# Optimization experiments

Hardware: AMD Instinct MI355X
Metric: run time of the kernel (lower is better)

Reference implementation:

```python
import jax, jax.numpy as jnp
import numpy as np

T, D_IN, D, H, A = 8192, 2048, 512, 512, 18  # seq_len, obs_dim, dense_size, cell_size, action_size


def setup_inputs() -> dict:
    key = jax.random.key(0)
    ks = jax.random.split(key, 12)
    g = lambda k, sh, s: (jax.random.normal(k, sh, jnp.float32) * s)
    return {
        "x": g(ks[0], (T, D_IN), 1.0),
        "prev_hidden": jnp.zeros((1, H), jnp.float32),
        "W1": g(ks[1], (D_IN, D), 0.02), "b1": jnp.zeros((D,), jnp.float32),
        "W2": g(ks[2], (D, D), 0.04),    "b2": jnp.zeros((D,), jnp.float32),
        "Wg": g(ks[3], (D, 3 * H), 0.04),   # GRU input kernel [D, 3H] (z|r|h)
        "Ug": g(ks[4], (H, 3 * H), 0.04),   # GRU recurrent kernel [H, 3H]
        "bg": jnp.zeros((2, 3 * H), jnp.float32),  # reset_after=True: input + recurrent bias
        "Wp": g(ks[5], (H, A), 0.05), "bp": jnp.zeros((A,), jnp.float32),
        "Wv": g(ks[6], (H, 1), 0.05), "bv": jnp.zeros((1,), jnp.float32),
    }


def reference(x, prev_hidden, W1, b1, W2, b2, Wg, Ug, bg, Wp, bp, Wv, bv):
    # MLP front-end (relu)
    z = jax.nn.relu(x @ W1 + b1)
    z = jax.nn.relu(z @ W2 + b2)
    # Precompute input projections for all timesteps: [T, 3H]
    X = z @ Wg + bg[0]
    b_rec = bg[1]

    def step(h, xt):  # h: [1,H], xt: [3H]
        rec = h @ Ug + b_rec                    # [1, 3H]
        xz, xr, xh = jnp.split(xt, 3)           # each [H]
        rz, rr, rh = jnp.split(rec, 3, axis=1)  # each [1, H]
        zt = jax.nn.sigmoid(xz + rz)
        rt = jax.nn.sigmoid(xr + rr)
        hh = jax.nn.sigmoid(xh + rt * rh)       # activation='sigmoid' (candidate)
        hn = zt * h + (1.0 - zt) * hh
        return hn, hn[0]

    hT, seq = jax.lax.scan(step, prev_hidden, X)  # seq: [T, H]
    policy = jax.nn.softmax(seq @ Wp + bp, axis=-1)
    value = seq @ Wv + bv
    return policy, value, hT
```

## Files before the change

### kernel.cpp

```cpp
#include <hip/hip_runtime.h>
#include <hip/hip_bf16.h>


#define T_STEPS 8192
#define DIN 2048
#define DD 512
#define HHH 512
#define AACT 18
#define H3 1536
#define NWG 32

typedef __attribute__((ext_vector_type(8))) short short8;
typedef __attribute__((ext_vector_type(4))) float f32x4;

__global__ void cast_f32_bf16(const float* __restrict__ in,
                              __hip_bfloat16* __restrict__ out, int n)
{
    int i = blockIdx.x * 256 + threadIdx.x;
    if (i < n) out[i] = __float2bfloat16(in[i]);
}

__global__ void init_ctl(int* ctl) { ctl[0] = 0; ctl[1] = 0; ctl[2] = 0; }

__global__ __launch_bounds__(256) void gemm_bf16(
    const float* __restrict__ A32, const __hip_bfloat16* __restrict__ A16,
    const __hip_bfloat16* __restrict__ B, const float* __restrict__ bias,
    __hip_bfloat16* __restrict__ Cb, float* __restrict__ Cf,
    int M, int N, int K, int relu)
{
    const int m0 = blockIdx.x * 64;
    const int n0 = blockIdx.y * 64;
    const int t  = threadIdx.x;
    const int wave = t >> 6;
    const int lane = t & 63;
    const int quad = lane >> 4;
    const int l16  = lane & 15;

    __shared__ __align__(16) __hip_bfloat16 As[64 * 40];
    __shared__ __align__(16) __hip_bfloat16 Bs[64 * 40];

    f32x4 acc[4];
#pragma unroll
    for (int c = 0; c < 4; ++c) acc[c] = (f32x4){0.f, 0.f, 0.f, 0.f};

    const int ar = t >> 2, akc = (t & 3) * 8;
    const int bk = t >> 3, bn  = (t & 7) * 8;

    for (int kb = 0; kb < K; kb += 32) {
        if (A32) {
            const float* src = A32 + (size_t)(m0 + ar) * K + kb + akc;
            float4 f0 = *(const float4*)(src);
            float4 f1 = *(const float4*)(src + 4);
            union { short8 v; __hip_bfloat16 h[8]; } u;
            u.h[0] = __float2bfloat16(f0.x); u.h[1] = __float2bfloat16(f0.y);
            u.h[2] = __float2bfloat16(f0.z); u.h[3] = __float2bfloat16(f0.w);
            u.h[4] = __float2bfloat16(f1.x); u.h[5] = __float2bfloat16(f1.y);
            u.h[6] = __float2bfloat16(f1.z); u.h[7] = __float2bfloat16(f1.w);
            *(short8*)&As[ar * 40 + akc] = u.v;
        } else {
            const __hip_bfloat16* src = A16 + (size_t)(m0 + ar) * K + kb + akc;
            *(short8*)&As[ar * 40 + akc] = *(const short8*)src;
        }
        {
            const __hip_bfloat16* src = B + (size_t)(kb + bk) * N + n0 + bn;
            short8 v = *(const short8*)src;
            const __hip_bfloat16* vh = (const __hip_bfloat16*)&v;
#pragma unroll
            for (int i = 0; i < 8; ++i) Bs[(bn + i) * 40 + bk] = vh[i];
        }
        __syncthreads();

        short8 a = *(const short8*)&As[(wave * 16 + l16) * 40 + quad * 8];
#pragma unroll
        for (int c = 0; c < 4; ++c) {
            short8 b = *(const short8*)&Bs[(c * 16 + l16) * 40 + quad * 8];
            acc[c] = __builtin_amdgcn_mfma_f32_16x16x32_bf16(a, b, acc[c], 0, 0, 0);
        }
        __syncthreads();
    }

#pragma unroll
    for (int c = 0; c < 4; ++c) {
        const int col = n0 + c * 16 + l16;
        const float bb = bias ? bias[col] : 0.f;
#pragma unroll
        for (int r = 0; r < 4; ++r) {
            const int row = m0 + wave * 16 + quad * 4 + r;
            float v = acc[c][r] + bb;
            if (relu) v = fmaxf(v, 0.f);
            if (Cb) Cb[(size_t)row * N + col] = __float2bfloat16(v);
            if (Cf) Cf[(size_t)row * N + col] = v;
        }
    }
}

template <int CTRL>
__device__ __forceinline__ float dpp_red_add(float x)
{
    int sh = __builtin_amdgcn_update_dpp(0, __float_as_int(x), CTRL, 0xF, 0xF, true);
    return x + __int_as_float(sh);
}

__device__ __forceinline__ void wg_barrier_lds_only()
{
    asm volatile("s_waitcnt lgkmcnt(0)" ::: "memory");
    __builtin_amdgcn_s_barrier();
    asm volatile("" ::: "memory");
}

__global__ __launch_bounds__(256)
__attribute__((amdgpu_waves_per_eu(1, 1)))
void scan_kernel(
    const float* __restrict__ X,
    const float* __restrict__ Ug,
    const float* __restrict__ bg,
    const float* __restrict__ h0,
    float* __restrict__ seq,
    unsigned long long* __restrict__ hbuf,
    float* __restrict__ hT,
    int* __restrict__ ctl)
{
    const int t  = threadIdx.x;
    const int wg = blockIdx.x;
    const int jl = t >> 4;
    const int kp = t & 15;
    const int j  = wg * 16 + jl;
    const int k0 = kp * 32;

    __shared__ __align__(16) float h_lds[2][16 * 36];
    __shared__ int wg_abort;
    if (t == 0) wg_abort = 0;

    float wz[32], wr[32], wh[32];
#pragma unroll
    for (int m = 0; m < 32; ++m) {
        const float* row = Ug + (size_t)(k0 + m) * H3;
        wz[m] = row[j];
        wr[m] = row[512 + j];
        wh[m] = row[1024 + j];
    }
#pragma unroll
    for (int m = 0; m < 32; ++m) {
        asm volatile("" : "+a"(wz[m]), "+a"(wr[m]), "+a"(wh[m]));
    }

    const float* brec = bg + H3;
    const float bz = brec[j], brr = brec[512 + j], bh = brec[1024 + j];
    float hj = h0[j];

    const int k1 = t, k2 = t + 256;
    const int la1 = (k1 >> 5) * 36 + (k1 & 31);
    const int la2 = (k2 >> 5) * 36 + (k2 & 31);

    float xz = 0.f, xr = 0.f, xh = 0.f;
    if (kp == 0) { xz = X[j]; xr = X[512 + j]; xh = X[1024 + j]; }

    for (int s = 0; s < T_STEPS; ++s) {
        float* hl = h_lds[s & 1];

        float nxz = 0.f, nxr = 0.f, nxh = 0.f;
        if (kp == 0 && s + 1 < T_STEPS) {
            const float* Xs = X + (size_t)(s + 1) * H3;
            nxz = Xs[j]; nxr = Xs[512 + j]; nxh = Xs[1024 + j];
        }

        if (s == 0) {
            hl[la1] = h0[k1];
            hl[la2] = h0[k2];
        } else {
            const unsigned long long* src = hbuf + ((size_t)(s & 1) << 9);
            unsigned long long v1 = 0, v2 = 0;
            unsigned long long a1 = __hip_atomic_load(src + k1, __ATOMIC_RELAXED, __HIP_MEMORY_SCOPE_AGENT);
            unsigned long long a2 = __hip_atomic_load(src + k2, __ATOMIC_RELAXED, __HIP_MEMORY_SCOPE_AGENT);
            asm volatile("" ::: "memory");
            __builtin_amdgcn_s_sleep(4);
            asm volatile("" ::: "memory");
            unsigned long long b1 = __hip_atomic_load(src + k1, __ATOMIC_RELAXED, __HIP_MEMORY_SCOPE_AGENT);
            unsigned long long b2 = __hip_atomic_load(src + k2, __ATOMIC_RELAXED, __HIP_MEMORY_SCOPE_AGENT);
            bool ok1 = false, ok2 = false;
            int guard = 0;
            for (;;) {
                if (!ok1 && (unsigned)(a1 >> 32) == (unsigned)s) { v1 = a1; ok1 = true; }
                if (!ok2 && (unsigned)(a2 >> 32) == (unsigned)s) { v2 = a2; ok2 = true; }
                if (ok1 && ok2) break;
                if (!ok1) a1 = __hip_atomic_load(src + k1, __ATOMIC_RELAXED, __HIP_MEMORY_SCOPE_AGENT);
                if (!ok2) a2 = __hip_atomic_load(src + k2, __ATOMIC_RELAXED, __HIP_MEMORY_SCOPE_AGENT);
                if (!ok1 && (unsigned)(b1 >> 32) == (unsigned)s) { v1 = b1; ok1 = true; }
                if (!ok2 && (unsigned)(b2 >> 32) == (unsigned)s) { v2 = b2; ok2 = true; }
                if (ok1 && ok2) break;
                if (!ok1) b1 = __hip_atomic_load(src + k1, __ATOMIC_RELAXED, __HIP_MEMORY_SCOPE_AGENT);
                if (!ok2) b2 = __hip_atomic_load(src + k2, __ATOMIC_RELAXED, __HIP_MEMORY_SCOPE_AGENT);
                if ((++guard & 511) == 0) {
                    int ab = __hip_atomic_load(ctl + 2, __ATOMIC_RELAXED,
                                               __HIP_MEMORY_SCOPE_AGENT);
                    if (ab || guard > (1 << 16)) {
                        wg_abort = 1;
                        __hip_atomic_store(ctl + 2, 1, __ATOMIC_RELAXED,
                                           __HIP_MEMORY_SCOPE_AGENT);
                        break;
                    }
                }
            }
            hl[la1] = __uint_as_float((unsigned)v1);
            hl[la2] = __uint_as_float((unsigned)v2);
        }
        wg_barrier_lds_only();
        if (wg_abort) return;

        float accz = 0.f, accr = 0.f, acch = 0.f;
        const float* hb = &hl[kp * 36];
#pragma unroll
        for (int m = 0; m < 32; m += 4) {
            float4 hv = *(const float4*)(hb + m);
            accz = fmaf(hv.x, wz[m    ], accz);
            accz = fmaf(hv.y, wz[m + 1], accz);
            accz = fmaf(hv.z, wz[m + 2], accz);
            accz = fmaf(hv.w, wz[m + 3], accz);
            accr = fmaf(hv.x, wr[m    ], accr);
            accr = fmaf(hv.y, wr[m + 1], accr);
            accr = fmaf(hv.z, wr[m + 2], accr);
            accr = fmaf(hv.w, wr[m + 3], accr);
            acch = fmaf(hv.x, wh[m    ], acch);
            acch = fmaf(hv.y, wh[m + 1], acch);
            acch = fmaf(hv.z, wh[m + 2], acch);
            acch = fmaf(hv.w, wh[m + 3], acch);
        }
        accz = dpp_red_add<0x108>(accz);
        accr = dpp_red_add<0x108>(accr);
        acch = dpp_red_add<0x108>(acch);
        accz = dpp_red_add<0x104>(accz);
        accr = dpp_red_add<0x104>(accr);
        acch = dpp_red_add<0x104>(acch);
        accz = dpp_red_add<0x102>(accz);
        accr = dpp_red_add<0x102>(accr);
        acch = dpp_red_add<0x102>(acch);
        accz = dpp_red_add<0x101>(accz);
        accr = dpp_red_add<0x101>(accr);
        acch = dpp_red_add<0x101>(acch);

        if (kp == 0) {
            const float rz = accz + bz, rr = accr + brr, rh = acch + bh;
            const float zt = 1.f / (1.f + __expf(-(xz + rz)));
            const float rt = 1.f / (1.f + __expf(-(xr + rr)));
            const float hc = 1.f / (1.f + __expf(-(xh + rt * rh)));
            const float hn = zt * hj + (1.f - zt) * hc;
            hj = hn;
            unsigned long long pk =
                ((unsigned long long)(unsigned)(s + 1) << 32) | (unsigned)__float_as_uint(hn);
            __hip_atomic_store(hbuf + (size_t)(((s + 1) & 1) << 9) + j, pk,
                               __ATOMIC_RELAXED, __HIP_MEMORY_SCOPE_AGENT);
            seq[(size_t)s * HHH + j] = hn;
            if (s == T_STEPS - 1) hT[j] = hn;
        }
        xz = nxz; xr = nxr; xh = nxh;
    }
}

__global__ __launch_bounds__(64) void heads_kernel(
    const float* __restrict__ seq, const float* __restrict__ Wp,
    const float* __restrict__ bp, const float* __restrict__ Wv,
    const float* __restrict__ bv, float* __restrict__ pol,
    float* __restrict__ val)
{
    const int s = blockIdx.x;
    const int l = threadIdx.x;
    const float* h = seq + (size_t)s * HHH;

    float acc[19];
#pragma unroll
    for (int jj = 0; jj < 19; ++jj) acc[jj] = 0.f;

#pragma unroll
    for (int kk = 0; kk < 8; ++kk) {
        const int k = kk * 64 + l;
        const float hv = h[k];
        const float* wrow = Wp + (size_t)k * AACT;
#pragma unroll
        for (int jj = 0; jj < AACT; ++jj) acc[jj] = fmaf(hv, wrow[jj], acc[jj]);
        acc[18] = fmaf(hv, Wv[k], acc[18]);
    }
#pragma unroll
    for (int jj = 0; jj < 19; ++jj) {
        float v = acc[jj];
#pragma unroll
        for (int off = 32; off; off >>= 1) v += __shfl_down(v, off, 64);
        acc[jj] = v;
    }
    if (l == 0) {
        float lg[18], mx = -1e30f;
#pragma unroll
        for (int jj = 0; jj < AACT; ++jj) { lg[jj] = acc[jj] + bp[jj]; mx = fmaxf(mx, lg[jj]); }
        float sum = 0.f;
#pragma unroll
        for (int jj = 0; jj < AACT; ++jj) { lg[jj] = __expf(lg[jj] - mx); sum += lg[jj]; }
        const float inv = 1.f / sum;
#pragma unroll
        for (int jj = 0; jj < AACT; ++jj) pol[(size_t)s * AACT + jj] = lg[jj] * inv;
        val[s] = acc[18] + bv[0];
    }
}

extern "C" void kernel_launch(void* const* d_in, const int* in_sizes, int n_in,
                              void* d_out, int out_size, void* d_ws, size_t ws_size,
                              hipStream_t stream)
{
    const float* x  = (const float*)d_in[0];
    const float* h0 = (const float*)d_in[1];
    const float* W1 = (const float*)d_in[2];
    const float* b1 = (const float*)d_in[3];
    const float* W2 = (const float*)d_in[4];
    const float* b2 = (const float*)d_in[5];
    const float* Wg = (const float*)d_in[6];
    const float* Ug = (const float*)d_in[7];
    const float* bg = (const float*)d_in[8];
    const float* Wp = (const float*)d_in[9];
    const float* bp = (const float*)d_in[10];
    const float* Wv = (const float*)d_in[11];
    const float* bv = (const float*)d_in[12];

    char* ws = (char*)d_ws;
    __hip_bfloat16* W1b = (__hip_bfloat16*)(ws + 0);
    __hip_bfloat16* W2b = (__hip_bfloat16*)(ws + 2097152);
    __hip_bfloat16* Wgb = (__hip_bfloat16*)(ws + 2621440);
    __hip_bfloat16* z1b = (__hip_bfloat16*)(ws + 4194304);
    __hip_bfloat16* z2b = (__hip_bfloat16*)(ws + 12582912);
    float*          Xb  = (float*)(ws + 20971520);
    float*          seq = (float*)(ws + 71303168);
    unsigned long long* hbuf = (unsigned long long*)(ws + 88080384);
    int* ctl = (int*)(ws + 4194304);

    float* out = (float*)d_out;
    float* pol = out;
    float* val = out + (size_t)T_STEPS * AACT;
    float* hT  = out + (size_t)T_STEPS * AACT + T_STEPS;

    cast_f32_bf16<<<DIN * DD / 256, 256, 0, stream>>>(W1, W1b, DIN * DD);
    cast_f32_bf16<<<DD * DD / 256, 256, 0, stream>>>(W2, W2b, DD * DD);
    cast_f32_bf16<<<DD * H3 / 256, 256, 0, stream>>>(Wg, Wgb, DD * H3);

    dim3 blk(256);
    gemm_bf16<<<dim3(T_STEPS / 64, DD / 64), blk, 0, stream>>>(
        x, nullptr, W1b, b1, z1b, nullptr, T_STEPS, DD, DIN, 1);
    gemm_bf16<<<dim3(T_STEPS / 64, DD / 64), blk, 0, stream>>>(
        nullptr, z1b, W2b, b2, z2b, nullptr, T_STEPS, DD, DD, 1);
    gemm_bf16<<<dim3(T_STEPS / 64, H3 / 64), blk, 0, stream>>>(
        nullptr, z2b, Wgb, bg, nullptr, Xb, T_STEPS, H3, DD, 0);

    init_ctl<<<1, 1, 0, stream>>>(ctl);
    scan_kernel<<<NWG, 256, 0, stream>>>(Xb, Ug, bg, h0, seq, hbuf, hT, ctl);

    heads_kernel<<<T_STEPS, 64, 0, stream>>>(seq, Wp, bp, Wv, bv, pol, val);
}
```

Measured before the change: 12.15 ms.

## Dedicate a publisher wave and split the polling load across three waves

```diff
diff --git a/kernel.cpp b/kernel.cpp
--- a/kernel.cpp
+++ b/kernel.cpp
@@ -126,8 +126,10 @@
     const int kp = t & 15;
     const int j  = wg * 16 + jl;
     const int k0 = kp * 32;
+    const int pl = t - 192;
 
     __shared__ __align__(16) float h_lds[2][16 * 36];
+    __shared__ unsigned long long hn_lds[16];
     __shared__ int wg_abort;
     if (t == 0) wg_abort = 0;
 
@@ -148,6 +150,12 @@
     const float bz = brec[j], brr = brec[512 + j], bh = brec[1024 + j];
     float hj = h0[j];
 
+    const int sA = t, sB = t + 192, sC = t + 384;
+    const int nsl = (t < 128) ? 3 : (t < 192 ? 2 : 0);
+    const int aA = (sA >> 5) * 36 + (sA & 31);
+    const int aB = (sB >> 5) * 36 + (sB & 31);
+    const int aC = (sC >> 5) * 36 + (sC & 31);
+
     const int k1 = t, k2 = t + 256;
     const int la1 = (k1 >> 5) * 36 + (k1 & 31);
     const int la2 = (k2 >> 5) * 36 + (k2 & 31);
@@ -158,39 +166,30 @@
     for (int s = 0; s < T_STEPS; ++s) {
         float* hl = h_lds[s & 1];
 
-        float nxz = 0.f, nxr = 0.f, nxh = 0.f;
-        if (kp == 0 && s + 1 < T_STEPS) {
-            const float* Xs = X + (size_t)(s + 1) * H3;
-            nxz = Xs[j]; nxr = Xs[512 + j]; nxh = Xs[1024 + j];
-        }
-
         if (s == 0) {
             hl[la1] = h0[k1];
             hl[la2] = h0[k2];
-        } else {
+            if (t < 16)
+                __hip_atomic_store(&hn_lds[t], 0ull, __ATOMIC_RELAXED,
+                                   __HIP_MEMORY_SCOPE_WORKGROUP);
+        } else if (nsl) {
             const unsigned long long* src = hbuf + ((size_t)(s & 1) << 9);
-            unsigned long long v1 = 0, v2 = 0;
-            unsigned long long a1 = __hip_atomic_load(src + k1, __ATOMIC_RELAXED, __HIP_MEMORY_SCOPE_AGENT);
-            unsigned long long a2 = __hip_atomic_load(src + k2, __ATOMIC_RELAXED, __HIP_MEMORY_SCOPE_AGENT);
-            asm volatile("" ::: "memory");
-            __builtin_amdgcn_s_sleep(4);
-            asm volatile("" ::: "memory");
-            unsigned long long b1 = __hip_atomic_load(src + k1, __ATOMIC_RELAXED, __HIP_MEMORY_SCOPE_AGENT);
-            unsigned long long b2 = __hip_atomic_load(src + k2, __ATOMIC_RELAXED, __HIP_MEMORY_SCOPE_AGENT);
-            bool ok1 = false, ok2 = false;
+            unsigned long long vA, vB, vC = 0;
+            bool okA = false, okB = false, okC = (nsl < 3);
+            vA = __hip_atomic_load(src + sA, __ATOMIC_RELAXED, __HIP_MEMORY_SCOPE_AGENT);
+            vB = __hip_atomic_load(src + sB, __ATOMIC_RELAXED, __HIP_MEMORY_SCOPE_AGENT);
+            if (nsl == 3)
+                vC = __hip_atomic_load(src + sC, __ATOMIC_RELAXED, __HIP_MEMORY_SCOPE_AGENT);
             int guard = 0;
             for (;;) {
-                if (!ok1 && (unsigned)(a1 >> 32) == (unsigned)s) { v1 = a1; ok1 = true; }
-                if (!ok2 && (unsigned)(a2 >> 32) == (unsigned)s) { v2 = a2; ok2 = true; }
-                if (ok1 && ok2) break;
-                if (!ok1) a1 = __hip_atomic_load(src + k1, __ATOMIC_RELAXED, __HIP_MEMORY_SCOPE_AGENT);
-                if (!ok2) a2 = __hip_atomic_load(src + k2, __ATOMIC_RELAXED, __HIP_MEMORY_SCOPE_AGENT);
-                if (!ok1 && (unsigned)(b1 >> 32) == (unsigned)s) { v1 = b1; ok1 = true; }
-                if (!ok2 && (unsigned)(b2 >> 32) == (unsigned)s) { v2 = b2; ok2 = true; }
-                if (ok1 && ok2) break;
-                if (!ok1) b1 = __hip_atomic_load(src + k1, __ATOMIC_RELAXED, __HIP_MEMORY_SCOPE_AGENT);
-                if (!ok2) b2 = __hip_atomic_load(src + k2, __ATOMIC_RELAXED, __HIP_MEMORY_SCOPE_AGENT);
-                if ((++guard & 511) == 0) {
+                if (!okA && (unsigned)(vA >> 32) == (unsigned)s) { hl[aA] = __uint_as_float((unsigned)vA); okA = true; }
+                if (!okB && (unsigned)(vB >> 32) == (unsigned)s) { hl[aB] = __uint_as_float((unsigned)vB); okB = true; }
+                if (!okC && (unsigned)(vC >> 32) == (unsigned)s) { hl[aC] = __uint_as_float((unsigned)vC); okC = true; }
+                if (okA && okB && okC) break;
+                if (!okA) vA = __hip_atomic_load(src + sA, __ATOMIC_RELAXED, __HIP_MEMORY_SCOPE_AGENT);
+                if (!okB) vB = __hip_atomic_load(src + sB, __ATOMIC_RELAXED, __HIP_MEMORY_SCOPE_AGENT);
+                if (!okC) vC = __hip_atomic_load(src + sC, __ATOMIC_RELAXED, __HIP_MEMORY_SCOPE_AGENT);
+                if ((++guard & 1023) == 0) {
                     int ab = __hip_atomic_load(ctl + 2, __ATOMIC_RELAXED,
                                                __HIP_MEMORY_SCOPE_AGENT);
                     if (ab || guard > (1 << 16)) {
@@ -201,11 +200,15 @@
                     }
                 }
             }
-            hl[la1] = __uint_as_float((unsigned)v1);
-            hl[la2] = __uint_as_float((unsigned)v2);
         }
         wg_barrier_lds_only();
         if (wg_abort) return;
+
+        float nxz = 0.f, nxr = 0.f, nxh = 0.f;
+        if (kp == 0 && s + 1 < T_STEPS) {
+            const float* Xs = X + (size_t)(s + 1) * H3;
+            nxz = Xs[j]; nxr = Xs[512 + j]; nxh = Xs[1024 + j];
+        }
 
         float accz = 0.f, accr = 0.f, acch = 0.f;
         const float* hb = &hl[kp * 36];
@@ -247,10 +250,27 @@
             hj = hn;
             unsigned long long pk =
                 ((unsigned long long)(unsigned)(s + 1) << 32) | (unsigned)__float_as_uint(hn);
-            __hip_atomic_store(hbuf + (size_t)(((s + 1) & 1) << 9) + j, pk,
+            __hip_atomic_store(&hn_lds[jl], pk, __ATOMIC_RELAXED,
+                               __HIP_MEMORY_SCOPE_WORKGROUP);
+        }
+
+        if (pl >= 0 && pl < 16) {
+            unsigned long long pk;
+            int guard = 0;
+            for (;;) {
+                pk = __hip_atomic_load(&hn_lds[pl], __ATOMIC_RELAXED,
+                                       __HIP_MEMORY_SCOPE_WORKGROUP);
+                if ((unsigned)(pk >> 32) == (unsigned)(s + 1)) break;
+                if ((++guard & 1023) == 0) {
+                    if (wg_abort || guard > (1 << 20)) break;
+                }
+            }
+            const int jj = wg * 16 + pl;
+            __hip_atomic_store(hbuf + ((size_t)((s + 1) & 1) << 9) + jj, pk,
                                __ATOMIC_RELAXED, __HIP_MEMORY_SCOPE_AGENT);
-            seq[(size_t)s * HHH + j] = hn;
-            if (s == T_STEPS - 1) hT[j] = hn;
+            const float hn = __uint_as_float((unsigned)pk);
+            seq[(size_t)s * HHH + jj] = hn;
+            if (s == T_STEPS - 1) hT[jj] = hn;
         }
         xz = nxz; xr = nxr; xh = nxh;
     }
```

New measurement: 14.34 ms. +18.0%, slower.
